# Performance work log

Measured on AMD Instinct MI355X. Metric: run time of the kernel, lower is better.

## Reference

```python
import jax, jax.numpy as jnp
import numpy as np

N_OUT = 100_000   # destination (output) nodes
N_IN = 200_000    # source nodes (x_feat rows); first N_OUT are the self/dst nodes
DEG = 16          # sample_count / fixed fan-out
E = N_OUT * DEG   # edges
D_IN = 128
D_OUT = 128


def setup_inputs() -> dict:
    key = jax.random.key(0)
    k1, k2, k3 = jax.random.split(key, 3)
    x_feat = jax.random.normal(k1, (N_IN, D_IN), dtype=jnp.float32)
    # MFG CSR with fixed fan-out DEG (what make_mfg_csr(sample_size=DEG) encodes)
    csr_row_ptr = jnp.arange(N_OUT + 1, dtype=jnp.int64) * DEG
    csr_col_ind = jax.random.randint(k2, (E,), 0, N_IN, dtype=jnp.int64)
    # Linear(2*D_IN, D_OUT) with xavier_uniform(gain for relu) weight
    gain = float(np.sqrt(2.0))
    fan_in, fan_out = 2 * D_IN, D_OUT
    bound = gain * float(np.sqrt(6.0 / (fan_in + fan_out)))
    W = jax.random.uniform(k3, (D_OUT, 2 * D_IN), dtype=jnp.float32,
                           minval=-bound, maxval=bound)
    lin_bias = jnp.zeros((D_OUT,), dtype=jnp.float32)
    bias = jnp.zeros((D_OUT,), dtype=jnp.float32)  # extra additive Parameter
    return {"x_feat": x_feat, "csr_row_ptr": csr_row_ptr,
            "csr_col_ind": csr_col_ind, "sample_count": DEG,
            "W": W, "lin_bias": lin_bias, "bias": bias}


def _segment_ids(row_ptr, n_edges):
    # seg[e] = destination row of edge e; handles empty rows via duplicate adds
    ones = jnp.zeros((n_edges,), dtype=jnp.int32).at[row_ptr[1:-1]].add(1)
    return jnp.cumsum(ones)


def reference(x_feat, csr_row_ptr, csr_col_ind, sample_count, W, lin_bias, bias):
    n_out = csr_row_ptr.shape[0] - 1
    n_edges = csr_col_ind.shape[0]
    seg = _segment_ids(csr_row_ptr, n_edges)
    # mean aggregation over sampled neighbors (cugraphops agg 'mean')
    gathered = x_feat[csr_col_ind]                          # [E, D_IN]
    summed = jax.ops.segment_sum(gathered, seg, num_segments=n_out)
    deg = (csr_row_ptr[1:] - csr_row_ptr[:-1]).astype(x_feat.dtype)
    mean_agg = summed / jnp.maximum(deg, 1.0)[:, None]      # [n_out, D_IN]
    # concat self (dst) features with aggregated features, then Linear
    x_agg = jnp.concatenate([x_feat[:n_out], mean_agg], axis=-1)  # [n_out, 2*D_IN]
    y = x_agg @ W.T + lin_bias + bias
    return y
```

## Files before the change

### kernel.cpp

```cpp
#include <hip/hip_runtime.h>
#include <hip/hip_bf16.h>

#define D 128
#define K2 256
#define NT 64
#define NTHREADS 256
#define AGG_LD 264
#define WT_LD 40

typedef __attribute__((ext_vector_type(8))) short bf16x8;
typedef __attribute__((ext_vector_type(4))) float f32x4;
typedef __attribute__((ext_vector_type(2))) float f32x2;

static __device__ __forceinline__ unsigned short f2bf(float f) {
    __hip_bfloat16 h = __float2bfloat16(f);
    return *reinterpret_cast<unsigned short*>(&h);
}

static __device__ __forceinline__ unsigned int f2q_manual(float f) {
    f = fminf(fmaxf(f, -448.f), 448.f);
    unsigned int u = __float_as_uint(f * 0x1.0p-120f);
    const unsigned int lsb = (u >> 20) & 1u;
    u += 0x7ffffu + lsb;
    return ((u >> 24) & 0x80u) | ((u >> 20) & 0x7fu);
}
static __device__ __forceinline__ float q2f_manual(unsigned int b) {
    const unsigned int bits = ((b & 0x80u) << 24) | ((b & 0x7fu) << 20);
    return __uint_as_float(bits) * 0x1.0p+120f;
}
static __device__ __forceinline__ unsigned int pack_fp8x4(float4 v) {
#if __has_builtin(__builtin_amdgcn_cvt_pk_fp8_f32)
    int lo = __builtin_amdgcn_cvt_pk_fp8_f32(v.x, v.y, 0, false);
    int q  = __builtin_amdgcn_cvt_pk_fp8_f32(v.z, v.w, lo, true);
    return (unsigned int)q;
#else
    return f2q_manual(v.x) | (f2q_manual(v.y) << 8) |
           (f2q_manual(v.z) << 16) | (f2q_manual(v.w) << 24);
#endif
}
static __device__ __forceinline__ f32x2 unpack_fp8x2(unsigned short v) {
#if __has_builtin(__builtin_amdgcn_cvt_pk_f32_fp8)
    return __builtin_amdgcn_cvt_pk_f32_fp8((int)(unsigned int)v, false);
#else
    f32x2 r;
    r[0] = q2f_manual(v & 0xffu);
    r[1] = q2f_manual((v >> 8) & 0xffu);
    return r;
#endif
}

__global__ __launch_bounds__(256)
void convert_all(const float* __restrict__ x, const float* __restrict__ W,
                 unsigned int* __restrict__ xq4,
                 uint2* __restrict__ xbs4,
                 uint2* __restrict__ wb4,
                 long n4x, long n4s, long n4w)
{
    const long gid = (long)blockIdx.x * blockDim.x + threadIdx.x;
    const long stride = (long)gridDim.x * blockDim.x;
    for (long t = gid; t < n4x; t += stride) {
        const float4 v = reinterpret_cast<const float4*>(x)[t];
        xq4[t] = pack_fp8x4(v);
        if (t < n4s) {
            uint2 p;
            p.x = (unsigned int)f2bf(v.x) | ((unsigned int)f2bf(v.y) << 16);
            p.y = (unsigned int)f2bf(v.z) | ((unsigned int)f2bf(v.w) << 16);
            xbs4[t] = p;
        }
    }
    for (long t = gid; t < n4w; t += stride) {
        const float4 v = reinterpret_cast<const float4*>(W)[t];
        uint2 p;
        p.x = (unsigned int)f2bf(v.x) | ((unsigned int)f2bf(v.y) << 16);
        p.y = (unsigned int)f2bf(v.z) | ((unsigned int)f2bf(v.w) << 16);
        wb4[t] = p;
    }
}

__global__ __launch_bounds__(NTHREADS, 3)
void sage_fp8(const unsigned char* __restrict__ xq,
              const unsigned short* __restrict__ xbs,
              const unsigned short* __restrict__ wb,
              const int* __restrict__ rp,
              const int* __restrict__ ci,
              const float* __restrict__ lb,
              const float* __restrict__ bb,
              float* __restrict__ y,
              int n_out)
{
    __shared__ unsigned short aggB[NT][AGG_LD];
    __shared__ unsigned short wtT[D][WT_LD];
    __shared__ int rpls[NT + 1];
    __shared__ int cils[NT * 16];

    const int tid   = threadIdx.x;
    const int wave  = tid >> 6;
    const int lane  = tid & 63;
    const int node0 = blockIdx.x * NT;
    const int nt_act = min(NT, n_out - node0);

    if (tid <= nt_act) rpls[tid] = rp[node0 + tid];
    __syncthreads();
    const int e_base = rpls[0];
    const int e_cnt  = rpls[nt_act] - e_base;
    const bool fits  = (e_cnt <= NT * 16);
    if (fits) {
        for (int i = tid; i < e_cnt; i += NTHREADS) cils[i] = ci[e_base + i];
    }
    __syncthreads();

    for (int t = 0; t < 16; t += 2) {
        const int nn0 = wave * 16 + t;
        if (nn0 >= nt_act) break;
        const int nn1 = nn0 + 1;
        const bool has1 = (nn1 < nt_act);

        const int s0 = rpls[nn0] - e_base;
        const int d0 = rpls[nn0 + 1] - e_base - s0;
        const int s1 = has1 ? rpls[nn1] - e_base : 0;
        const int d1 = has1 ? rpls[nn1 + 1] - e_base - s1 : 0;

        const unsigned int self0 = *reinterpret_cast<const unsigned int*>(
            &xbs[(size_t)(node0 + nn0) * D + lane * 2]);
        unsigned int self1 = 0;
        if (has1) self1 = *reinterpret_cast<const unsigned int*>(
            &xbs[(size_t)(node0 + nn1) * D + lane * 2]);

        float a0x = 0.f, a0y = 0.f, a1x = 0.f, a1y = 0.f;
        if (fits && has1 && d0 == 16 && d1 == 16) {
            int idx0[16], idx1[16];
            #pragma unroll
            for (int u = 0; u < 16; ++u) { idx0[u] = cils[s0 + u]; idx1[u] = cils[s1 + u]; }
            #pragma unroll
            for (int u = 0; u < 16; ++u) {
                const unsigned short v0 = *reinterpret_cast<const unsigned short*>(
                    &xq[(size_t)idx0[u] * D + lane * 2]);
                const unsigned short v1 = *reinterpret_cast<const unsigned short*>(
                    &xq[(size_t)idx1[u] * D + lane * 2]);
                const f32x2 e0 = unpack_fp8x2(v0);
                const f32x2 e1 = unpack_fp8x2(v1);
                a0x += e0[0]; a0y += e0[1];
                a1x += e1[0]; a1y += e1[1];
            }
        } else {
            for (int u = 0; u < d0; ++u) {
                const int c = fits ? cils[s0 + u] : ci[e_base + s0 + u];
                const f32x2 e0 = unpack_fp8x2(*reinterpret_cast<const unsigned short*>(
                    &xq[(size_t)c * D + lane * 2]));
                a0x += e0[0]; a0y += e0[1];
            }
            for (int u = 0; u < d1; ++u) {
                const int c = fits ? cils[s1 + u] : ci[e_base + s1 + u];
                const f32x2 e1 = unpack_fp8x2(*reinterpret_cast<const unsigned short*>(
                    &xq[(size_t)c * D + lane * 2]));
                a1x += e1[0]; a1y += e1[1];
            }
        }

        const float inv0 = 1.0f / (float)max(d0, 1);
        *reinterpret_cast<unsigned int*>(&aggB[nn0][lane * 2]) = self0;
        *reinterpret_cast<unsigned int*>(&aggB[nn0][D + lane * 2]) =
            (unsigned int)f2bf(a0x * inv0) | ((unsigned int)f2bf(a0y * inv0) << 16);
        if (has1) {
            const float inv1 = 1.0f / (float)max(d1, 1);
            *reinterpret_cast<unsigned int*>(&aggB[nn1][lane * 2]) = self1;
            *reinterpret_cast<unsigned int*>(&aggB[nn1][D + lane * 2]) =
                (unsigned int)f2bf(a1x * inv1) | ((unsigned int)f2bf(a1y * inv1) << 16);
        }
    }

    const int n15 = lane & 15;
    const int g   = lane >> 4;

    f32x4 acc[8];
    #pragma unroll
    for (int f = 0; f < 8; ++f) acc[f] = (f32x4){0.f, 0.f, 0.f, 0.f};

    for (int k0 = 0; k0 < K2; k0 += 32) {
        #pragma unroll
        for (int j = 0; j < 2; ++j) {
            const int idx = j * 256 + tid;
            const int o   = idx >> 2;
            const int q   = idx & 3;
            *reinterpret_cast<uint4*>(&wtT[o][q * 8]) =
                *reinterpret_cast<const uint4*>(&wb[(size_t)o * K2 + k0 + q * 8]);
        }
        __syncthreads();

        const bf16x8 a = *reinterpret_cast<const bf16x8*>(
            &aggB[wave * 16 + n15][k0 + g * 8]);
        #pragma unroll
        for (int f = 0; f < 8; ++f) {
            const bf16x8 b = *reinterpret_cast<const bf16x8*>(&wtT[f * 16 + n15][g * 8]);
            acc[f] = __builtin_amdgcn_mfma_f32_16x16x32_bf16(a, b, acc[f], 0, 0, 0);
        }
        __syncthreads();
    }

    const int mbase = node0 + wave * 16 + g * 4;
    #pragma unroll
    for (int f = 0; f < 8; ++f) {
        const int col  = f * 16 + n15;
        const float bs = lb[col] + bb[col];
        #pragma unroll
        for (int r = 0; r < 4; ++r) {
            const int row = mbase + r;
            if (row < n_out)
                y[(size_t)row * D + col] = acc[f][r] + bs;
        }
    }
}

__global__ __launch_bounds__(NTHREADS, 3)
void sage_fused3(const float* __restrict__ x,
                 const int* __restrict__ rp,
                 const int* __restrict__ ci,
                 const float* __restrict__ W,
                 const float* __restrict__ lb,
                 const float* __restrict__ bb,
                 float* __restrict__ y,
                 int n_out)
{
    __shared__ unsigned short aggB[NT][AGG_LD];
    __shared__ unsigned short wtT[D][32];
    __shared__ int rpls[NT + 1];
    __shared__ int cilsF[NT * 16];

    const int tid   = threadIdx.x;
    const int wave  = tid >> 6;
    const int lane  = tid & 63;
    const int node0 = blockIdx.x * NT;
    const int nt_act = min(NT, n_out - node0);

    if (tid <= nt_act) rpls[tid] = rp[node0 + tid];
    __syncthreads();
    const int e_base = rpls[0];
    const int e_cnt  = rpls[nt_act] - e_base;
    const bool fits  = (e_cnt <= NT * 16);
    if (fits) {
        for (int i = tid; i < e_cnt; i += NTHREADS) cilsF[i] = ci[e_base + i];
    }
    __syncthreads();

    for (int t = 0; t < 16; ++t) {
        const int nn = wave * 16 + t;
        if (nn >= nt_act) break;
        const int node = node0 + nn;
        const float2 self =
            *reinterpret_cast<const float2*>(&x[(size_t)node * D + lane * 2]);
        const int s  = rpls[nn] - e_base;
        const int dg = rpls[nn + 1] - e_base - s;
        float ax = 0.f, ay = 0.f;
        for (int u = 0; u < dg; ++u) {
            const int c = fits ? cilsF[s + u] : ci[e_base + s + u];
            const float2 v = *reinterpret_cast<const float2*>(
                &x[(size_t)c * D + lane * 2]);
            ax += v.x; ay += v.y;
        }
        const float inv = 1.0f / (float)max(dg, 1);
        *reinterpret_cast<unsigned int*>(&aggB[nn][lane * 2]) =
            (unsigned int)f2bf(self.x) | ((unsigned int)f2bf(self.y) << 16);
        *reinterpret_cast<unsigned int*>(&aggB[nn][D + lane * 2]) =
            (unsigned int)f2bf(ax * inv) | ((unsigned int)f2bf(ay * inv) << 16);
    }

    const int n15 = lane & 15;
    const int g   = lane >> 4;
    f32x4 acc[8];
    #pragma unroll
    for (int f = 0; f < 8; ++f) acc[f] = (f32x4){0.f, 0.f, 0.f, 0.f};

    for (int k0 = 0; k0 < K2; k0 += 32) {
        #pragma unroll
        for (int j = 0; j < 4; ++j) {
            const int idx = j * 256 + tid;
            const int o   = idx >> 3;
            const int c   = idx & 7;
            const float4 w = *reinterpret_cast<const float4*>(
                &W[(size_t)o * K2 + k0 + c * 4]);
            const unsigned int lo = (unsigned int)f2bf(w.x) | ((unsigned int)f2bf(w.y) << 16);
            const unsigned int hi = (unsigned int)f2bf(w.z) | ((unsigned int)f2bf(w.w) << 16);
            *reinterpret_cast<uint2*>(&wtT[o][c * 4]) = make_uint2(lo, hi);
        }
        __syncthreads();
        const bf16x8 a = *reinterpret_cast<const bf16x8*>(
            &aggB[wave * 16 + n15][k0 + g * 8]);
        #pragma unroll
        for (int f = 0; f < 8; ++f) {
            const bf16x8 b = *reinterpret_cast<const bf16x8*>(&wtT[f * 16 + n15][g * 8]);
            acc[f] = __builtin_amdgcn_mfma_f32_16x16x32_bf16(a, b, acc[f], 0, 0, 0);
        }
        __syncthreads();
    }

    const int mbase = node0 + wave * 16 + g * 4;
    #pragma unroll
    for (int f = 0; f < 8; ++f) {
        const int col  = f * 16 + n15;
        const float bs = lb[col] + bb[col];
        #pragma unroll
        for (int r = 0; r < 4; ++r) {
            const int row = mbase + r;
            if (row < n_out)
                y[(size_t)row * D + col] = acc[f][r] + bs;
        }
    }
}

extern "C" void kernel_launch(void* const* d_in, const int* in_sizes, int n_in,
                              void* d_out, int out_size, void* d_ws, size_t ws_size,
                              hipStream_t stream)
{
    const float* x  = (const float*)d_in[0];
    const int*   rp = (const int*)d_in[1];
    const int*   ci = (const int*)d_in[2];
    const float* W  = (const float*)d_in[4];
    const float* lb = (const float*)d_in[5];
    const float* bb = (const float*)d_in[6];
    float* y = (float*)d_out;

    const int n_out = in_sizes[1] - 1;
    const int grid  = (n_out + NT - 1) / NT;

    const size_t n_x = (size_t)in_sizes[0];
    const size_t n_w = (size_t)in_sizes[4];
    const size_t xq_bytes  = n_x;
    const size_t xbs_bytes = (size_t)n_out * D * 2;
    const size_t wb_bytes  = n_w * 2;
    const size_t need = xq_bytes + xbs_bytes + wb_bytes;

    if (ws_size >= need) {
        unsigned char*  xq  = (unsigned char*)d_ws;
        unsigned short* xbs = (unsigned short*)((char*)d_ws + xq_bytes);
        unsigned short* wb  = (unsigned short*)((char*)d_ws + xq_bytes + xbs_bytes);
        hipLaunchKernelGGL(convert_all, dim3(2048), dim3(256), 0, stream,
                           x, W, (unsigned int*)xq, (uint2*)xbs, (uint2*)wb,
                           (long)(n_x >> 2), (long)(((size_t)n_out * D) >> 2),
                           (long)(n_w >> 2));
        hipLaunchKernelGGL(sage_fp8, dim3(grid), dim3(NTHREADS), 0, stream,
                           xq, xbs, wb, rp, ci, lb, bb, y, n_out);
    } else {
        hipLaunchKernelGGL(sage_fused3, dim3(grid), dim3(NTHREADS), 0, stream,
                           x, rp, ci, W, lb, bb, y, n_out);
    }
}
```

Measured before the change: 87.44 us.

## Widen fp8 gathers, load self features directly into MFMA registers, enlarge weight chunks

The fp8 gather is restructured so each half-wave handles one node and loads 4 fp8 bytes per lane instead of 2, halving the number of gather instructions per row. Self features are now read straight from global memory into MFMA A-fragments rather than staged through shared memory. As a result the aggregation tile covers only the mean half, and weights are staged in 64-wide K chunks, which halves the barrier count. The smaller LDS footprint allows an occupancy hint of 4 blocks. The risk is more register pressure from the held self fragments and fewer independent gather streams per lane.

```diff
diff --git a/kernel.cpp b/kernel.cpp
--- a/kernel.cpp
+++ b/kernel.cpp
@@ -5,8 +5,8 @@
 #define K2 256
 #define NT 64
 #define NTHREADS 256
-#define AGG_LD 264
-#define WT_LD 40
+#define AGM_LD 136
+#define WT_LD 68
 
 typedef __attribute__((ext_vector_type(8))) short bf16x8;
 typedef __attribute__((ext_vector_type(4))) float f32x4;
@@ -38,14 +38,18 @@
            (f2q_manual(v.z) << 16) | (f2q_manual(v.w) << 24);
 #endif
 }
-static __device__ __forceinline__ f32x2 unpack_fp8x2(unsigned short v) {
+static __device__ __forceinline__ f32x2 unpack_fp8_lo(unsigned int v) {
 #if __has_builtin(__builtin_amdgcn_cvt_pk_f32_fp8)
-    return __builtin_amdgcn_cvt_pk_f32_fp8((int)(unsigned int)v, false);
+    return __builtin_amdgcn_cvt_pk_f32_fp8((int)v, false);
 #else
-    f32x2 r;
-    r[0] = q2f_manual(v & 0xffu);
-    r[1] = q2f_manual((v >> 8) & 0xffu);
-    return r;
+    f32x2 r; r[0] = q2f_manual(v & 0xffu); r[1] = q2f_manual((v >> 8) & 0xffu); return r;
+#endif
+}
+static __device__ __forceinline__ f32x2 unpack_fp8_hi(unsigned int v) {
+#if __has_builtin(__builtin_amdgcn_cvt_pk_f32_fp8)
+    return __builtin_amdgcn_cvt_pk_f32_fp8((int)v, true);
+#else
+    f32x2 r; r[0] = q2f_manual((v >> 16) & 0xffu); r[1] = q2f_manual((v >> 24) & 0xffu); return r;
 #endif
 }
 
@@ -77,18 +81,18 @@
     }
 }
 
-__global__ __launch_bounds__(NTHREADS, 3)
-void sage_fp8(const unsigned char* __restrict__ xq,
-              const unsigned short* __restrict__ xbs,
-              const unsigned short* __restrict__ wb,
-              const int* __restrict__ rp,
-              const int* __restrict__ ci,
-              const float* __restrict__ lb,
-              const float* __restrict__ bb,
-              float* __restrict__ y,
-              int n_out)
+__global__ __launch_bounds__(NTHREADS, 4)
+void sage_fp8b(const unsigned char* __restrict__ xq,
+               const unsigned short* __restrict__ xbs,
+               const unsigned short* __restrict__ wb,
+               const int* __restrict__ rp,
+               const int* __restrict__ ci,
+               const float* __restrict__ lb,
+               const float* __restrict__ bb,
+               float* __restrict__ y,
+               int n_out)
 {
-    __shared__ unsigned short aggB[NT][AGG_LD];
+    __shared__ unsigned short aggM[NT][AGM_LD];
     __shared__ unsigned short wtT[D][WT_LD];
     __shared__ int rpls[NT + 1];
     __shared__ int cils[NT * 16];
@@ -109,90 +113,96 @@
     }
     __syncthreads();
 
-    for (int t = 0; t < 16; t += 2) {
-        const int nn0 = wave * 16 + t;
-        if (nn0 >= nt_act) break;
-        const int nn1 = nn0 + 1;
-        const bool has1 = (nn1 < nt_act);
-
-        const int s0 = rpls[nn0] - e_base;
-        const int d0 = rpls[nn0 + 1] - e_base - s0;
-        const int s1 = has1 ? rpls[nn1] - e_base : 0;
-        const int d1 = has1 ? rpls[nn1 + 1] - e_base - s1 : 0;
-
-        const unsigned int self0 = *reinterpret_cast<const unsigned int*>(
-            &xbs[(size_t)(node0 + nn0) * D + lane * 2]);
-        unsigned int self1 = 0;
-        if (has1) self1 = *reinterpret_cast<const unsigned int*>(
-            &xbs[(size_t)(node0 + nn1) * D + lane * 2]);
-
-        float a0x = 0.f, a0y = 0.f, a1x = 0.f, a1y = 0.f;
+    const int nsel = lane >> 5;
+    const int dg4  = (lane & 31) * 4;
+
+    for (int p = 0; p < 8; ++p) {
+        const int n0 = wave * 16 + p * 2;
+        if (n0 >= nt_act) break;
+        const bool has1 = (n0 + 1 < nt_act);
+
+        const int s0 = rpls[n0] - e_base;
+        const int d0 = rpls[n0 + 1] - e_base - s0;
+        int s1 = s0, d1 = d0;
+        if (has1) { s1 = rpls[n0 + 1] - e_base; d1 = rpls[n0 + 2] - e_base - s1; }
+
+        const int  my_n   = n0 + nsel;
+        const int  my_s   = nsel ? s1 : s0;
+        const int  my_d   = nsel ? d1 : d0;
+        const bool active = (nsel == 0) || has1;
+
+        float a0 = 0.f, a1 = 0.f, a2 = 0.f, a3 = 0.f;
         if (fits && has1 && d0 == 16 && d1 == 16) {
-            int idx0[16], idx1[16];
+            int idx[16];
             #pragma unroll
-            for (int u = 0; u < 16; ++u) { idx0[u] = cils[s0 + u]; idx1[u] = cils[s1 + u]; }
+            for (int u = 0; u < 16; ++u) idx[u] = cils[my_s + u];
             #pragma unroll
             for (int u = 0; u < 16; ++u) {
-                const unsigned short v0 = *reinterpret_cast<const unsigned short*>(
-                    &xq[(size_t)idx0[u] * D + lane * 2]);
-                const unsigned short v1 = *reinterpret_cast<const unsigned short*>(
-                    &xq[(size_t)idx1[u] * D + lane * 2]);
-                const f32x2 e0 = unpack_fp8x2(v0);
-                const f32x2 e1 = unpack_fp8x2(v1);
-                a0x += e0[0]; a0y += e0[1];
-                a1x += e1[0]; a1y += e1[1];
+                const unsigned int v = *reinterpret_cast<const unsigned int*>(
+                    &xq[(size_t)idx[u] * D + dg4]);
+                const f32x2 lo = unpack_fp8_lo(v);
+                const f32x2 hi = unpack_fp8_hi(v);
+                a0 += lo[0]; a1 += lo[1]; a2 += hi[0]; a3 += hi[1];
             }
-        } else {
-            for (int u = 0; u < d0; ++u) {
-                const int c = fits ? cils[s0 + u] : ci[e_base + s0 + u];
-                const f32x2 e0 = unpack_fp8x2(*reinterpret_cast<const unsigned short*>(
-                    &xq[(size_t)c * D + lane * 2]));
-                a0x += e0[0]; a0y += e0[1];
+        } else if (active) {
+            for (int u = 0; u < my_d; ++u) {
+                const int c = fits ? cils[my_s + u] : ci[e_base + my_s + u];
+                const unsigned int v = *reinterpret_cast<const unsigned int*>(
+                    &xq[(size_t)c * D + dg4]);
+                const f32x2 lo = unpack_fp8_lo(v);
+                const f32x2 hi = unpack_fp8_hi(v);
+                a0 += lo[0]; a1 += lo[1]; a2 += hi[0]; a3 += hi[1];
             }
-            for (int u = 0; u < d1; ++u) {
-                const int c = fits ? cils[s1 + u] : ci[e_base + s1 + u];
-                const f32x2 e1 = unpack_fp8x2(*reinterpret_cast<const unsigned short*>(
-                    &xq[(size_t)c * D + lane * 2]));
-                a1x += e1[0]; a1y += e1[1];
-            }
-        }
-
-        const float inv0 = 1.0f / (float)max(d0, 1);
-        *reinterpret_cast<unsigned int*>(&aggB[nn0][lane * 2]) = self0;
-        *reinterpret_cast<unsigned int*>(&aggB[nn0][D + lane * 2]) =
-            (unsigned int)f2bf(a0x * inv0) | ((unsigned int)f2bf(a0y * inv0) << 16);
-        if (has1) {
-            const float inv1 = 1.0f / (float)max(d1, 1);
-            *reinterpret_cast<unsigned int*>(&aggB[nn1][lane * 2]) = self1;
-            *reinterpret_cast<unsigned int*>(&aggB[nn1][D + lane * 2]) =
-                (unsigned int)f2bf(a1x * inv1) | ((unsigned int)f2bf(a1y * inv1) << 16);
+        }
+        if (active) {
+            const float inv = 1.0f / (float)max(my_d, 1);
+            uint2 pk;
+            pk.x = (unsigned int)f2bf(a0 * inv) | ((unsigned int)f2bf(a1 * inv) << 16);
+            pk.y = (unsigned int)f2bf(a2 * inv) | ((unsigned int)f2bf(a3 * inv) << 16);
+            *reinterpret_cast<uint2*>(&aggM[my_n][dg4]) = pk;
         }
     }
 
     const int n15 = lane & 15;
     const int g   = lane >> 4;
 
+    const int arow = min(node0 + wave * 16 + n15, n_out - 1);
+    bf16x8 aself[4];
+    #pragma unroll
+    for (int c = 0; c < 4; ++c)
+        aself[c] = *reinterpret_cast<const bf16x8*>(
+            &xbs[(size_t)arow * D + c * 32 + g * 8]);
+
     f32x4 acc[8];
     #pragma unroll
     for (int f = 0; f < 8; ++f) acc[f] = (f32x4){0.f, 0.f, 0.f, 0.f};
 
-    for (int k0 = 0; k0 < K2; k0 += 32) {
-        #pragma unroll
-        for (int j = 0; j < 2; ++j) {
-            const int idx = j * 256 + tid;
-            const int o   = idx >> 2;
-            const int q   = idx & 3;
-            *reinterpret_cast<uint4*>(&wtT[o][q * 8]) =
-                *reinterpret_cast<const uint4*>(&wb[(size_t)o * K2 + k0 + q * 8]);
+    #pragma unroll
+    for (int ch = 0; ch < 4; ++ch) {
+        const int k0 = ch * 64;
+        #pragma unroll
+        for (int j = 0; j < 8; ++j) {
+            const int flat = j * 256 + tid;
+            const int o    = flat >> 4;
+            const int q    = flat & 15;
+            *reinterpret_cast<uint2*>(&wtT[o][q * 4]) =
+                *reinterpret_cast<const uint2*>(&wb[(size_t)o * K2 + k0 + q * 4]);
         }
         __syncthreads();
 
-        const bf16x8 a = *reinterpret_cast<const bf16x8*>(
-            &aggB[wave * 16 + n15][k0 + g * 8]);
-        #pragma unroll
-        for (int f = 0; f < 8; ++f) {
-            const bf16x8 b = *reinterpret_cast<const bf16x8*>(&wtT[f * 16 + n15][g * 8]);
-            acc[f] = __builtin_amdgcn_mfma_f32_16x16x32_bf16(a, b, acc[f], 0, 0, 0);
+        #pragma unroll
+        for (int sub = 0; sub < 2; ++sub) {
+            const int kk = k0 + sub * 32;
+            const bf16x8 a = (kk < 128)
+                ? aself[ch * 2 + sub]
+                : *reinterpret_cast<const bf16x8*>(
+                      &aggM[wave * 16 + n15][(kk - 128) + g * 8]);
+            #pragma unroll
+            for (int f = 0; f < 8; ++f) {
+                const bf16x8 b = *reinterpret_cast<const bf16x8*>(
+                    &wtT[f * 16 + n15][sub * 32 + g * 8]);
+                acc[f] = __builtin_amdgcn_mfma_f32_16x16x32_bf16(a, b, acc[f], 0, 0, 0);
+            }
         }
         __syncthreads();
     }
@@ -211,6 +221,7 @@
     }
 }
 
+#define AGG_LDF 264
 __global__ __launch_bounds__(NTHREADS, 3)
 void sage_fused3(const float* __restrict__ x,
                  const int* __restrict__ rp,
@@ -221,8 +232,8 @@
                  float* __restrict__ y,
                  int n_out)
 {
-    __shared__ unsigned short aggB[NT][AGG_LD];
-    __shared__ unsigned short wtT[D][32];
+    __shared__ unsigned short aggB[NT][AGG_LDF];
+    __shared__ unsigned short wtTF[D][32];
     __shared__ int rpls[NT + 1];
     __shared__ int cilsF[NT * 16];
 
@@ -280,14 +291,14 @@
                 &W[(size_t)o * K2 + k0 + c * 4]);
             const unsigned int lo = (unsigned int)f2bf(w.x) | ((unsigned int)f2bf(w.y) << 16);
             const unsigned int hi = (unsigned int)f2bf(w.z) | ((unsigned int)f2bf(w.w) << 16);
-            *reinterpret_cast<uint2*>(&wtT[o][c * 4]) = make_uint2(lo, hi);
+            *reinterpret_cast<uint2*>(&wtTF[o][c * 4]) = make_uint2(lo, hi);
         }
         __syncthreads();
         const bf16x8 a = *reinterpret_cast<const bf16x8*>(
             &aggB[wave * 16 + n15][k0 + g * 8]);
         #pragma unroll
         for (int f = 0; f < 8; ++f) {
-            const bf16x8 b = *reinterpret_cast<const bf16x8*>(&wtT[f * 16 + n15][g * 8]);
+            const bf16x8 b = *reinterpret_cast<const bf16x8*>(&wtTF[f * 16 + n15][g * 8]);
             acc[f] = __builtin_amdgcn_mfma_f32_16x16x32_bf16(a, b, acc[f], 0, 0, 0);
         }
         __syncthreads();
@@ -337,7 +348,7 @@
                            x, W, (unsigned int*)xq, (uint2*)xbs, (uint2*)wb,
                            (long)(n_x >> 2), (long)(((size_t)n_out * D) >> 2),
                            (long)(n_w >> 2));
-        hipLaunchKernelGGL(sage_fp8, dim3(grid), dim3(NTHREADS), 0, stream,
+        hipLaunchKernelGGL(sage_fp8b, dim3(grid), dim3(NTHREADS), 0, stream,
                            xq, xbs, wb, rp, ci, lb, bb, y, n_out);
     } else {
         hipLaunchKernelGGL(sage_fused3, dim3(grid), dim3(NTHREADS), 0, stream,
```

Measured after the change: 78.93 us. 9.7% less time.
